# Kernel tuning notes

Hardware: AMD Instinct MI355X
Metric: run time of the kernel (lower is better)

Reference implementation:

```python
import jax, jax.numpy as jnp
import numpy as np

V, S, D, H, F, LYR, NLAB, B = 30522, 512, 768, 12, 3072, 12, 2, 16
DH = D // H
EPS = 1e-5


def layer_norm(x, scale, bias):
    mu = jnp.mean(x, axis=-1, keepdims=True)
    var = jnp.mean((x - mu) ** 2, axis=-1, keepdims=True)
    return (x - mu) * jax.lax.rsqrt(var + EPS) * scale + bias


def setup_inputs() -> dict:
    key = jax.random.key(0)
    ks = jax.random.split(key, 16)
    sc = 0.02
    inp = {
        "input_ids": jax.random.randint(ks[0], (B, S), 0, V),
        "token_emb": jax.random.normal(ks[1], (V, D), jnp.float32) * sc,
        "pos_emb": jax.random.normal(ks[2], (S, D), jnp.float32) * sc,
        "emb_ln_s": jnp.ones((D,), jnp.float32),
        "emb_ln_b": jnp.zeros((D,), jnp.float32),
        "wq": jax.random.normal(ks[3], (LYR, H, D, DH), jnp.float32) * sc,
        "wk": jax.random.normal(ks[4], (LYR, H, D, DH), jnp.float32) * sc,
        "wv": jax.random.normal(ks[5], (LYR, H, D, DH), jnp.float32) * sc,
        "wo": jax.random.normal(ks[6], (LYR, D, D), jnp.float32) * sc,
        "wo_b": jnp.zeros((LYR, D), jnp.float32),
        "ln1_s": jnp.ones((LYR, D), jnp.float32),
        "ln1_b": jnp.zeros((LYR, D), jnp.float32),
        "ln2_s": jnp.ones((LYR, D), jnp.float32),
        "ln2_b": jnp.zeros((LYR, D), jnp.float32),
        "ff1_w": jax.random.normal(ks[7], (LYR, D, F), jnp.float32) * sc,
        "ff1_b": jnp.zeros((LYR, F), jnp.float32),
        "ff2_w": jax.random.normal(ks[8], (LYR, F, D), jnp.float32) * sc,
        "ff2_b": jnp.zeros((LYR, D), jnp.float32),
        "final_ln_s": jnp.ones((D,), jnp.float32),
        "final_ln_b": jnp.zeros((D,), jnp.float32),
        "clf_w": jax.random.normal(ks[9], (D, NLAB), jnp.float32) * sc,
        "clf_b": jnp.zeros((NLAB,), jnp.float32),
    }
    return inp


def _encoder_block(x, wq, wk, wv, wo, wo_b, ln1_s, ln1_b, ln2_s, ln2_b,
                   ff1_w, ff1_b, ff2_w, ff2_b):
    # pre-LN attention with residual
    h = layer_norm(x, ln1_s, ln1_b)
    q = jnp.einsum("bsd,hde->bhse", h, wq)
    k = jnp.einsum("bsd,hde->bhse", h, wk)
    v = jnp.einsum("bsd,hde->bhse", h, wv)
    scores = jnp.einsum("bhse,bhte->bhst", q, k) / jnp.sqrt(jnp.float32(DH))
    # NOTE: source uses log_softmax (quirk), faithfully preserved
    w = jax.nn.log_softmax(scores, axis=-1)
    ctx = jnp.einsum("bhst,bhte->bhse", w, v)
    ctx = ctx.transpose(0, 2, 1, 3).reshape(x.shape[0], x.shape[1], D)
    x = x + ctx @ wo + wo_b
    # pre-LN FFN with residual (exact GELU as in torch nn.GELU)
    h2 = layer_norm(x, ln2_s, ln2_b)
    ff = jax.nn.gelu(h2 @ ff1_w + ff1_b, approximate=False) @ ff2_w + ff2_b
    return x + ff


def reference(input_ids, token_emb, pos_emb, emb_ln_s, emb_ln_b,
              wq, wk, wv, wo, wo_b, ln1_s, ln1_b, ln2_s, ln2_b,
              ff1_w, ff1_b, ff2_w, ff2_b, final_ln_s, final_ln_b,
              clf_w, clf_b):
    x = token_emb[input_ids] + pos_emb[None, :, :]
    x = layer_norm(x, emb_ln_s, emb_ln_b)
    for l in range(LYR):
        x = _encoder_block(x, wq[l], wk[l], wv[l], wo[l], wo_b[l],
                           ln1_s[l], ln1_b[l], ln2_s[l], ln2_b[l],
                           ff1_w[l], ff1_b[l], ff2_w[l], ff2_b[l])
    x = layer_norm(x, final_ln_s, final_ln_b)
    cls = x[:, 0, :]
    return cls @ clf_w + clf_b
```

## Files before the change

### kernel.cpp

```cpp
#include <hip/hip_runtime.h>
#include <hip/hip_bf16.h>
#include <math.h>

typedef __bf16 bf16_t;
typedef __attribute__((ext_vector_type(8))) __bf16 bf16x8;
typedef __attribute__((ext_vector_type(4))) float f32x4;

typedef const __attribute__((address_space(1))) void av1_void;
typedef __attribute__((address_space(3))) void av3_void;

#define DEV static __device__ __forceinline__

DEV void gload16(const void* g, void* l) {
  __builtin_amdgcn_global_load_lds((av1_void*)g, (av3_void*)l, 16, 0, 0);
}

DEV float bsum3(float v, float* red) {
#pragma unroll
  for (int o = 32; o > 0; o >>= 1) v += __shfl_xor(v, o, 64);
  __syncthreads();
  if ((threadIdx.x & 63) == 0) red[threadIdx.x >> 6] = v;
  __syncthreads();
  return red[0] + red[1] + red[2];
}

__global__ __launch_bounds__(192) void k_embed(
    const int* __restrict__ ids, const float* __restrict__ tok,
    const float* __restrict__ pos, const float* __restrict__ gam,
    const float* __restrict__ bet, const float* __restrict__ gam2,
    const float* __restrict__ bet2, float* __restrict__ x,
    bf16_t* __restrict__ h) {
  __shared__ float red[3];
  int row = blockIdx.x;
  int s = row & 511;
  int t = threadIdx.x;
  int id = ids[row];
  const float4 tv = *(const float4*)&tok[(size_t)id * 768 + t * 4];
  const float4 pv = *(const float4*)&pos[(size_t)s * 768 + t * 4];
  float v[4] = {tv.x + pv.x, tv.y + pv.y, tv.z + pv.z, tv.w + pv.w};
  float tot = bsum3(v[0] + v[1] + v[2] + v[3], red);
  float mu = tot * (1.f / 768.f);
  float sq = 0.f;
#pragma unroll
  for (int u = 0; u < 4; ++u) { float d = v[u] - mu; sq += d * d; }
  float var = bsum3(sq, red) * (1.f / 768.f);
  float rstd = rsqrtf(var + 1e-5f);
  const float4 g4 = *(const float4*)&gam[t * 4];
  const float4 b4 = *(const float4*)&bet[t * 4];
  float o[4];
  o[0] = (v[0] - mu) * rstd * g4.x + b4.x;
  o[1] = (v[1] - mu) * rstd * g4.y + b4.y;
  o[2] = (v[2] - mu) * rstd * g4.z + b4.z;
  o[3] = (v[3] - mu) * rstd * g4.w + b4.w;
  float4 ov = {o[0], o[1], o[2], o[3]};
  *(float4*)&x[(size_t)row * 768 + t * 4] = ov;
  float tot2 = bsum3(o[0] + o[1] + o[2] + o[3], red);
  float mu2 = tot2 * (1.f / 768.f);
  float sq2 = 0.f;
#pragma unroll
  for (int u = 0; u < 4; ++u) { float d = o[u] - mu2; sq2 += d * d; }
  float var2 = bsum3(sq2, red) * (1.f / 768.f);
  float rstd2 = rsqrtf(var2 + 1e-5f);
  const float4 G = *(const float4*)&gam2[t * 4];
  const float4 Bb = *(const float4*)&bet2[t * 4];
  union { bf16_t ob[4]; uint2 u2; } pk;
  pk.ob[0] = (bf16_t)((o[0] - mu2) * rstd2 * G.x + Bb.x);
  pk.ob[1] = (bf16_t)((o[1] - mu2) * rstd2 * G.y + Bb.y);
  pk.ob[2] = (bf16_t)((o[2] - mu2) * rstd2 * G.z + Bb.z);
  pk.ob[3] = (bf16_t)((o[3] - mu2) * rstd2 * G.w + Bb.w);
  *(uint2*)&h[(size_t)row * 768 + t * 4] = pk.u2;
}

__global__ __launch_bounds__(256) void k_ln(
    const float* __restrict__ xin, bf16_t* __restrict__ hout,
    const float* __restrict__ gam, const float* __restrict__ bet) {
  int row = blockIdx.x * 4 + (threadIdx.x >> 6);
  int lane = threadIdx.x & 63;
  const float* xr = xin + (size_t)row * 768 + lane * 12;
  float4 a = *(const float4*)&xr[0];
  float4 b = *(const float4*)&xr[4];
  float4 c = *(const float4*)&xr[8];
  float v[12] = {a.x, a.y, a.z, a.w, b.x, b.y, b.z, b.w, c.x, c.y, c.z, c.w};
  float sm = 0.f;
#pragma unroll
  for (int u = 0; u < 12; ++u) sm += v[u];
#pragma unroll
  for (int o = 32; o > 0; o >>= 1) sm += __shfl_xor(sm, o, 64);
  float mu = sm * (1.f / 768.f);
  float sq = 0.f;
#pragma unroll
  for (int u = 0; u < 12; ++u) { float d = v[u] - mu; sq += d * d; }
#pragma unroll
  for (int o = 32; o > 0; o >>= 1) sq += __shfl_xor(sq, o, 64);
  float rstd = rsqrtf(sq * (1.f / 768.f) + 1e-5f);
  const float4 ga = *(const float4*)&gam[lane * 12];
  const float4 gb = *(const float4*)&gam[lane * 12 + 4];
  const float4 gc = *(const float4*)&gam[lane * 12 + 8];
  const float4 ba = *(const float4*)&bet[lane * 12];
  const float4 bb = *(const float4*)&bet[lane * 12 + 4];
  const float4 bc = *(const float4*)&bet[lane * 12 + 8];
  float g[12] = {ga.x, ga.y, ga.z, ga.w, gb.x, gb.y, gb.z, gb.w,
                 gc.x, gc.y, gc.z, gc.w};
  float be[12] = {ba.x, ba.y, ba.z, ba.w, bb.x, bb.y, bb.z, bb.w,
                  bc.x, bc.y, bc.z, bc.w};
  union { bf16_t o[12]; uint2 u2[3]; } pk;
#pragma unroll
  for (int u = 0; u < 12; ++u)
    pk.o[u] = (bf16_t)((v[u] - mu) * rstd * g[u] + be[u]);
  bf16_t* hr = hout + (size_t)row * 768 + lane * 12;
#pragma unroll
  for (int u = 0; u < 3; ++u) *(uint2*)&hr[u * 4] = pk.u2[u];
}

__global__ __launch_bounds__(256) void k_convT(
    const float* __restrict__ in, size_t in_slice, bf16_t* __restrict__ out,
    size_t out_slice, int N, int K) {
  __shared__ float tbuf[32][33];
  int slice = blockIdx.z;
  const float* ip = in + (size_t)slice * in_slice;
  bf16_t* op = out + (size_t)slice * out_slice;
  int n0 = blockIdx.x * 32, k0 = blockIdx.y * 32;
  int c = threadIdx.x & 31, r8 = threadIdx.x >> 5;
#pragma unroll
  for (int i = 0; i < 4; ++i) {
    int rr = r8 + i * 8;
    tbuf[rr][c] = ip[(size_t)(k0 + rr) * N + n0 + c];
  }
  __syncthreads();
#pragma unroll
  for (int i = 0; i < 4; ++i) {
    int rr = r8 + i * 8;
    op[(size_t)(n0 + rr) * K + k0 + c] = (bf16_t)tbuf[c][rr];
  }
}

__global__ __launch_bounds__(256) void k_convT3(
    const float* __restrict__ wq, const float* __restrict__ wk,
    const float* __restrict__ wv, bf16_t* __restrict__ out,
    size_t in_lstride, size_t out_lstride) {
  __shared__ float tbuf[32][33];
  int z = blockIdx.z;
  int l = z / 36, r = z % 36;
  int which = r / 12, head = r % 12;
  const float* ip = (which == 0 ? wq : which == 1 ? wk : wv) +
                    (size_t)l * in_lstride + (size_t)head * 768 * 64;
  bf16_t* op = out + (size_t)l * out_lstride + (size_t)which * 768 * 768 +
               (size_t)head * 64 * 768;
  int n0 = blockIdx.x * 32, k0 = blockIdx.y * 32;
  int c = threadIdx.x & 31, r8 = threadIdx.x >> 5;
#pragma unroll
  for (int i = 0; i < 4; ++i) {
    int rr = r8 + i * 8;
    tbuf[rr][c] = ip[(size_t)(k0 + rr) * 64 + n0 + c];
  }
  __syncthreads();
#pragma unroll
  for (int i = 0; i < 4; ++i) {
    int rr = r8 + i * 8;
    op[(size_t)(n0 + rr) * 768 + k0 + c] = (bf16_t)tbuf[c][rr];
  }
}

template <int EPI>
__global__ __launch_bounds__(256) void k_gemm1(
    const bf16_t* __restrict__ A, int lda, const bf16_t* __restrict__ Bt,
    int ldb, int K, float* __restrict__ Cf, bf16_t* __restrict__ Cb, int ldc,
    const float* __restrict__ bias, int gx) {
  __shared__ __attribute__((aligned(16))) bf16_t As[128 * 64];
  __shared__ __attribute__((aligned(16))) bf16_t Bs[128 * 64];
  const int nwg = gridDim.x;
  const int bid = blockIdx.x;
  const int cpx = nwg >> 3;
  const int swz = (bid & 7) * cpx + (bid >> 3);
  const int bx = swz % gx, by = swz / gx;
  const int m0 = by << 7, n0 = bx << 7;
  const int tid = threadIdx.x;
  const int lane = tid & 63, w = tid >> 6;
  const int wm = w >> 1, wn = w & 1;
  const int r = lane & 15, g4 = lane >> 4;

  f32x4 acc[4][4];
#pragma unroll
  for (int m = 0; m < 4; ++m)
#pragma unroll
    for (int n = 0; n < 4; ++n)
#pragma unroll
      for (int e = 0; e < 4; ++e) acc[m][n][e] = 0.f;

  const bf16_t* pa[4];
  const bf16_t* pb[4];
  char* la[4];
  char* lb[4];
#pragma unroll
  for (int u = 0; u < 4; ++u) {
    int s = u * 256 + tid;
    int row = s >> 3;
    int c = (s & 7) ^ (row & 7);
    pa[u] = A + (size_t)(m0 + row) * lda + c * 8;
    pb[u] = Bt + (size_t)(n0 + row) * ldb + c * 8;
    la[u] = (char*)As + (size_t)(u * 256 + (w << 6)) * 16;
    lb[u] = (char*)Bs + (size_t)(u * 256 + (w << 6)) * 16;
  }

  const int NT = K >> 6;
  for (int t = 0; t < NT; ++t) {
    const int k0 = t << 6;
#pragma unroll
    for (int u = 0; u < 4; ++u) gload16(pa[u] + k0, la[u]);
#pragma unroll
    for (int u = 0; u < 4; ++u) gload16(pb[u] + k0, lb[u]);
    __syncthreads();

#pragma unroll
    for (int kk = 0; kk < 2; ++kk) {
      bf16x8 af[4], bb[4];
#pragma unroll
      for (int m = 0; m < 4; ++m) {
        int row = wm * 64 + m * 16 + r;
        af[m] = *(const bf16x8*)&As[row * 64 +
                                    (((kk << 2) + g4) ^ (row & 7)) * 8];
      }
#pragma unroll
      for (int n = 0; n < 4; ++n) {
        int row = wn * 64 + n * 16 + r;
        bb[n] = *(const bf16x8*)&Bs[row * 64 +
                                    (((kk << 2) + g4) ^ (row & 7)) * 8];
      }
#pragma unroll
      for (int m = 0; m < 4; ++m)
#pragma unroll
        for (int n = 0; n < 4; ++n)
          acc[m][n] = __builtin_amdgcn_mfma_f32_16x16x32_bf16(af[m], bb[n],
                                                              acc[m][n], 0, 0, 0);
    }
    __syncthreads();
  }

#pragma unroll
  for (int m = 0; m < 4; ++m) {
#pragma unroll
    for (int n = 0; n < 4; ++n) {
      int col = n0 + wn * 64 + n * 16 + r;
      float bv = 0.f;
      if constexpr (EPI != 0) bv = bias[col];
#pragma unroll
      for (int j = 0; j < 4; ++j) {
        int row = m0 + wm * 64 + m * 16 + g4 * 4 + j;
        float v = acc[m][n][j];
        if constexpr (EPI == 0) {
          Cb[(size_t)row * ldc + col] = (bf16_t)v;
        } else if constexpr (EPI == 1) {
          size_t o = (size_t)row * ldc + col;
          Cf[o] += v + bv;
        } else {
          float tt = v + bv;
          float ge = 0.5f * tt * (1.f + erff(tt * 0.70710678118f));
          Cb[(size_t)row * ldc + col] = (bf16_t)ge;
        }
      }
    }
  }
}

template <int EPI>
__global__ __launch_bounds__(256) void k_gemm3h(
    const bf16_t* __restrict__ A, int lda, const bf16_t* __restrict__ Bt,
    int ldb, int K, float* __restrict__ Cf, bf16_t* __restrict__ Cb, int ldc,
    const float* __restrict__ bias, int gx) {
  __shared__ __attribute__((aligned(16))) bf16_t As[3][64 * 32];
  __shared__ __attribute__((aligned(16))) bf16_t Bs[3][128 * 32];
  const int nwg = gridDim.x;
  const int bid = blockIdx.x;
  const int cpx = nwg >> 3;
  const int swz = (bid & 7) * cpx + (bid >> 3);
  const int bx = swz % gx, by = swz / gx;
  const int m0 = by << 6, n0 = bx << 7;
  const int tid = threadIdx.x;
  const int lane = tid & 63, w = tid >> 6;
  const int wm = w >> 1, wn = w & 1;
  const int r = lane & 15, g4 = lane >> 4;

  f32x4 acc[2][4];
#pragma unroll
  for (int m = 0; m < 2; ++m)
#pragma unroll
    for (int n = 0; n < 4; ++n)
#pragma unroll
      for (int e = 0; e < 4; ++e) acc[m][n][e] = 0.f;

  const bf16_t* pa0;
  const bf16_t* pb[2];
  uint32_t loa, lob[2];
  {
    int s = tid;
    int row = s >> 2;
    int c = (s & 3) ^ ((row >> 1) & 3);
    pa0 = A + (size_t)(m0 + row) * lda + c * 8;
    loa = (uint32_t)(w << 6) * 16;
#pragma unroll
    for (int u = 0; u < 2; ++u) {
      int sb = u * 256 + tid;
      int rowb = sb >> 2;
      int cb = (sb & 3) ^ ((rowb >> 1) & 3);
      pb[u] = Bt + (size_t)(n0 + rowb) * ldb + cb * 8;
      lob[u] = (uint32_t)(u * 256 + (w << 6)) * 16;
    }
  }

  const int NT = K >> 5;
  auto STAGE = [&](int t, int bufi) {
    int k0 = (t < NT ? t : NT - 1) << 5;
    gload16(pa0 + k0, (char*)&As[bufi][0] + loa);
#pragma unroll
    for (int u = 0; u < 2; ++u) gload16(pb[u] + k0, (char*)&Bs[bufi][0] + lob[u]);
  };

  STAGE(0, 0);
  STAGE(1, 1);
  int bi = 0, si = 2;
  const int co = (g4 ^ ((r >> 1) & 3)) << 3;
  for (int t = 0; t < NT; ++t) {
    asm volatile("s_waitcnt vmcnt(3)" ::: "memory");
    asm volatile("s_barrier" ::: "memory");
    bf16x8 af[2], bb[4];
#pragma unroll
    for (int m = 0; m < 2; ++m) {
      int row = wm * 32 + m * 16 + r;
      af[m] = *(const bf16x8*)&As[bi][row * 32 + co];
    }
#pragma unroll
    for (int n = 0; n < 4; ++n) {
      int row = wn * 64 + n * 16 + r;
      bb[n] = *(const bf16x8*)&Bs[bi][row * 32 + co];
    }
#pragma unroll
    for (int m = 0; m < 2; ++m)
#pragma unroll
      for (int n = 0; n < 4; ++n)
        acc[m][n] = __builtin_amdgcn_mfma_f32_16x16x32_bf16(af[m], bb[n],
                                                            acc[m][n], 0, 0, 0);
    asm volatile("s_barrier" ::: "memory");
    STAGE(t + 2, si);
    si = bi;
    bi = (bi == 2) ? 0 : bi + 1;
  }
  asm volatile("s_waitcnt vmcnt(0)" ::: "memory");

#pragma unroll
  for (int m = 0; m < 2; ++m) {
#pragma unroll
    for (int n = 0; n < 4; ++n) {
      int col = n0 + wn * 64 + n * 16 + r;
      float bv = 0.f;
      if constexpr (EPI != 0) bv = bias[col];
#pragma unroll
      for (int j = 0; j < 4; ++j) {
        int row = m0 + wm * 32 + m * 16 + g4 * 4 + j;
        float v = acc[m][n][j];
        if constexpr (EPI == 0) {
          Cb[(size_t)row * ldc + col] = (bf16_t)v;
        } else if constexpr (EPI == 1) {
          size_t o = (size_t)row * ldc + col;
          Cf[o] += v + bv;
        } else {
          float tt = v + bv;
          float ge = 0.5f * tt * (1.f + erff(tt * 0.70710678118f));
          Cb[(size_t)row * ldc + col] = (bf16_t)ge;
        }
      }
    }
  }
}

__global__ __launch_bounds__(512) void k_attn(const bf16_t* __restrict__ qkv,
                                              bf16_t* __restrict__ ctx) {
  __shared__ __attribute__((aligned(16))) bf16_t Ks[512 * 64];
  __shared__ __attribute__((aligned(16))) float Vs[128 * 64];
  __shared__ __attribute__((aligned(16))) bf16_t Qs[2][128 * 64];
  __shared__ __attribute__((aligned(16))) bf16_t Mt[64 * 64];
  __shared__ float svp[8 * 64];
  __shared__ float svs[64];

  int bh = blockIdx.x;
  int b = bh / 12, hh = bh % 12;
  int tid = threadIdx.x, lane = tid & 63, w = tid >> 6;
  int r = lane & 15, g4 = lane >> 4;
  const bf16_t* qb = qkv + (size_t)b * 512 * 2304 + hh * 64;
  const bf16_t* kb = qb + 768;
  const bf16_t* vb = qb + 1536;

#pragma unroll
  for (int i = 0; i < 8; ++i) {
    int s = i * 512 + tid;
    int row = s >> 3;
    int c = (s & 7) ^ (row & 7);
    gload16(kb + (size_t)row * 2304 + c * 8,
            (char*)Ks + (size_t)(i * 512 + (w << 6)) * 16);
  }

  f32x4 macc[2];
#pragma unroll
  for (int jj = 0; jj < 2; ++jj)
#pragma unroll
    for (int e = 0; e < 4; ++e) macc[jj][e] = 0.f;
  float svacc = 0.f;
  const int e1hi = (lane >> 3), e1lo = (lane & 7);

  bf16x8 vreg[2];
  auto ldV = [&](int t0) {
#pragma unroll
    for (int i = 0; i < 2; ++i) {
      int cs = i * 512 + tid;
      int row = cs >> 3, col = (cs & 7) * 8;
      vreg[i] = *(const bf16x8*)(vb + (size_t)(t0 + row) * 2304 + col);
    }
  };
  auto wrV = [&]() {
#pragma unroll
    for (int i = 0; i < 2; ++i) {
      int cs = i * 512 + tid;
      int row = cs >> 3, col = (cs & 7) * 8;
      f32x4 v0, v1;
#pragma unroll
      for (int u = 0; u < 4; ++u) {
        v0[u] = (float)vreg[i][u];
        v1[u] = (float)vreg[i][u + 4];
      }
      *(f32x4*)&Vs[row * 64 + col] = v0;
      *(f32x4*)&Vs[row * 64 + col + 4] = v1;
    }
  };

  ldV(0);
  wrV();
  __syncthreads();

  for (int t0 = 0; t0 < 4; ++t0) {
    if (t0 < 3) ldV((t0 + 1) * 128);
#pragma unroll 8
    for (int tt = 0; tt < 128; ++tt) {
      int t = t0 * 128 + tt;
      float kv = (float)Ks[t * 64 + (((e1hi ^ (t & 7)) << 3) | e1lo)];
#pragma unroll
      for (int jj = 0; jj < 2; ++jj) {
        f32x4 vv = *(const f32x4*)&Vs[tt * 64 + w * 8 + jj * 4];
        macc[jj] += kv * vv;
      }
    }
#pragma unroll
    for (int q = 0; q < 16; ++q)
      svacc += Vs[((w << 4) + q) * 64 + lane];
    __syncthreads();
    if (t0 < 3) {
      wrV();
      __syncthreads();
    }
  }

#pragma unroll
  for (int jj = 0; jj < 2; ++jj)
#pragma unroll
    for (int u = 0; u < 4; ++u) {
      int e2 = w * 8 + jj * 4 + u;
      Mt[e2 * 64 + (((e1hi ^ (e2 & 7)) << 3) | e1lo)] =
          (bf16_t)(macc[jj][u] * 0.125f);
    }
  svp[w * 64 + lane] = svacc;
  __syncthreads();
  if (w == 0) {
    float s = 0.f;
#pragma unroll
    for (int u = 0; u < 8; ++u) s += svp[u * 64 + lane];
    svs[lane] = s;
  }

  auto stageQ = [&](int qc, int bufi) {
#pragma unroll
    for (int u = 0; u < 2; ++u) {
      int s = u * 512 + tid;
      int row = s >> 3;
      int c = (s & 7) ^ (row & 7);
      gload16(qb + (size_t)(qc * 128 + row) * 2304 + c * 8,
              (char*)&Qs[bufi][0] + (size_t)(u * 512 + (w << 6)) * 16);
    }
  };
  stageQ(0, 0);
  const int arow = w * 16 + r;

  for (int qc = 0; qc < 4; ++qc) {
    __syncthreads();
    if (qc < 3) stageQ(qc + 1, (qc + 1) & 1);
    const bf16_t* Qb = &Qs[qc & 1][0];

    f32x4 acc2[32];
#pragma unroll
    for (int n = 0; n < 32; ++n)
#pragma unroll
      for (int e = 0; e < 4; ++e) acc2[n][e] = 0.f;

#pragma unroll
    for (int kk = 0; kk < 2; ++kk) {
      bf16x8 aq = *(const bf16x8*)&Qb[arow * 64 +
                                      (((kk << 2) + g4) ^ (arow & 7)) * 8];
#pragma unroll
      for (int n = 0; n < 32; ++n) {
        int krow = n * 16 + r;
        bf16x8 bk = *(const bf16x8*)&Ks[krow * 64 +
                                        (((kk << 2) + g4) ^ (krow & 7)) * 8];
        acc2[n] = __builtin_amdgcn_mfma_f32_16x16x32_bf16(aq, bk, acc2[n], 0, 0, 0);
      }
    }

    float lse_j[4];
#pragma unroll
    for (int j = 0; j < 4; ++j) {
      float mx = -1e30f;
#pragma unroll
      for (int n = 0; n < 32; ++n) mx = fmaxf(mx, acc2[n][j] * 0.125f);
#pragma unroll
      for (int o = 1; o < 16; o <<= 1) mx = fmaxf(mx, __shfl_xor(mx, o, 64));
      float sm = 0.f;
#pragma unroll
      for (int n = 0; n < 32; ++n) sm += __expf(acc2[n][j] * 0.125f - mx);
#pragma unroll
      for (int o = 1; o < 16; o <<= 1) sm += __shfl_xor(sm, o, 64);
      lse_j[j] = mx + __logf(sm);
    }

    f32x4 acc3[4];
#pragma unroll
    for (int n = 0; n < 4; ++n)
#pragma unroll
      for (int e = 0; e < 4; ++e) acc3[n][e] = 0.f;
#pragma unroll
    for (int kk = 0; kk < 2; ++kk) {
      bf16x8 aq = *(const bf16x8*)&Qb[arow * 64 +
                                      (((kk << 2) + g4) ^ (arow & 7)) * 8];
#pragma unroll
      for (int n2 = 0; n2 < 4; ++n2) {
        int mrow = n2 * 16 + r;
        bf16x8 bm = *(const bf16x8*)&Mt[mrow * 64 +
                                        (((kk << 2) + g4) ^ (mrow & 7)) * 8];
        acc3[n2] = __builtin_amdgcn_mfma_f32_16x16x32_bf16(aq, bm, acc3[n2], 0, 0, 0);
      }
    }
#pragma unroll
    for (int n2 = 0; n2 < 4; ++n2) {
      int col = n2 * 16 + r;
      float svv = svs[col];
#pragma unroll
      for (int j = 0; j < 4; ++j) {
        int srow = qc * 128 + w * 16 + g4 * 4 + j;
        ctx[((size_t)(b * 512 + srow)) * 768 + hh * 64 + col] =
            (bf16_t)(acc3[n2][j] - lse_j[j] * svv);
      }
    }
  }
}

__global__ __launch_bounds__(192) void k_final(
    const float* __restrict__ x, const float* __restrict__ gam,
    const float* __restrict__ bet, const float* __restrict__ cw,
    const float* __restrict__ cb, float* __restrict__ out) {
  __shared__ float red[3];
  int b = blockIdx.x, t = threadIdx.x;
  const float* xr = x + (size_t)b * 512 * 768;
  const float4 xv = *(const float4*)&xr[t * 4];
  float v[4] = {xv.x, xv.y, xv.z, xv.w};
  float tot = bsum3(v[0] + v[1] + v[2] + v[3], red);
  float mu = tot * (1.f / 768.f);
  float sq = 0.f;
#pragma unroll
  for (int u = 0; u < 4; ++u) { float d = v[u] - mu; sq += d * d; }
  float var = bsum3(sq, red) * (1.f / 768.f);
  float rstd = rsqrtf(var + 1e-5f);
  const float4 g4 = *(const float4*)&gam[t * 4];
  const float4 b4 = *(const float4*)&bet[t * 4];
  float nv[4];
  nv[0] = (v[0] - mu) * rstd * g4.x + b4.x;
  nv[1] = (v[1] - mu) * rstd * g4.y + b4.y;
  nv[2] = (v[2] - mu) * rstd * g4.z + b4.z;
  nv[3] = (v[3] - mu) * rstd * g4.w + b4.w;
  const float4 wa = *(const float4*)&cw[t * 8];
  const float4 wb = *(const float4*)&cw[t * 8 + 4];
  float d0 = nv[0] * wa.x + nv[1] * wa.z + nv[2] * wb.x + nv[3] * wb.z;
  float d1 = nv[0] * wa.y + nv[1] * wa.w + nv[2] * wb.y + nv[3] * wb.w;
  d0 = bsum3(d0, red);
  d1 = bsum3(d1, red);
  if (t == 0) {
    out[b * 2 + 0] = d0 + cb[0];
    out[b * 2 + 1] = d1 + cb[1];
  }
}

static constexpr size_t OFF_X = 0;
static constexpr size_t OFF_H = OFF_X + 8192ull * 768 * 4;
static constexpr size_t OFF_QG = OFF_H + 8192ull * 768 * 2;
static constexpr size_t OFF_CTX = OFF_QG + 8192ull * 3072 * 2;
static constexpr size_t OFF_LSE = OFF_CTX + 8192ull * 768 * 2;
static constexpr size_t OFF_W = OFF_LSE + 192ull * 512 * 4;
static constexpr size_t WPL = 7077888;
static constexpr size_t WS_SMALL = OFF_W + WPL * 2;
static constexpr size_t WS_BIG = OFF_W + 12ull * WPL * 2;

extern "C" void kernel_launch(void* const* d_in, const int* in_sizes, int n_in,
                              void* d_out, int out_size, void* d_ws,
                              size_t ws_size, hipStream_t stream) {
  const int* ids = (const int*)d_in[0];
  const float* tok = (const float*)d_in[1];
  const float* pos = (const float*)d_in[2];
  const float* eln_s = (const float*)d_in[3];
  const float* eln_b = (const float*)d_in[4];
  const float* wq = (const float*)d_in[5];
  const float* wk = (const float*)d_in[6];
  const float* wv = (const float*)d_in[7];
  const float* wo = (const float*)d_in[8];
  const float* wo_b = (const float*)d_in[9];
  const float* ln1_s = (const float*)d_in[10];
  const float* ln1_b = (const float*)d_in[11];
  const float* ln2_s = (const float*)d_in[12];
  const float* ln2_b = (const float*)d_in[13];
  const float* ff1w = (const float*)d_in[14];
  const float* ff1b = (const float*)d_in[15];
  const float* ff2w = (const float*)d_in[16];
  const float* ff2b = (const float*)d_in[17];
  const float* fln_s = (const float*)d_in[18];
  const float* fln_b = (const float*)d_in[19];
  const float* cw = (const float*)d_in[20];
  const float* cb = (const float*)d_in[21];
  float* out = (float*)d_out;

  if (ws_size < WS_SMALL) return;
  const bool big = ws_size >= WS_BIG;

  char* ws = (char*)d_ws;
  float* x = (float*)(ws + OFF_X);
  bf16_t* h = (bf16_t*)(ws + OFF_H);
  bf16_t* qkv = (bf16_t*)(ws + OFF_QG);
  bf16_t* gbuf = (bf16_t*)(ws + OFF_QG);
  bf16_t* ctx = (bf16_t*)(ws + OFF_CTX);
  bf16_t* wT = (bf16_t*)(ws + OFF_W);

  k_embed<<<8192, 192, 0, stream>>>(ids, tok, pos, eln_s, eln_b,
                                    ln1_s, ln1_b, x, h);

  if (big) {
    k_convT3<<<dim3(2, 24, 432), 256, 0, stream>>>(wq, wk, wv, wT,
                                                   589824, WPL);
    k_convT<<<dim3(24, 24, 12), 256, 0, stream>>>(wo, 589824,
                                                  wT + 1769472, WPL, 768, 768);
    k_convT<<<dim3(96, 24, 12), 256, 0, stream>>>(ff1w, 2359296,
                                                  wT + 2359296, WPL, 3072, 768);
    k_convT<<<dim3(24, 96, 12), 256, 0, stream>>>(ff2w, 2359296,
                                                  wT + 4718592, WPL, 768, 3072);
  }

  for (int l = 0; l < 12; ++l) {
    bf16_t* wl = big ? wT + (size_t)l * WPL : wT;
    bf16_t* qkvT = wl;
    bf16_t* woT = wl + 1769472;
    bf16_t* ff1T = wl + 2359296;
    bf16_t* ff2T = wl + 4718592;

    if (l > 0)
      k_ln<<<2048, 256, 0, stream>>>(x, h, ln1_s + l * 768, ln1_b + l * 768);
    if (!big) {
      k_convT3<<<dim3(2, 24, 36), 256, 0, stream>>>(
          wq + (size_t)l * 589824, wk + (size_t)l * 589824,
          wv + (size_t)l * 589824, qkvT, 589824, 0);
      k_convT<<<dim3(24, 24, 1), 256, 0, stream>>>(wo + (size_t)l * 589824, 0,
                                                   woT, 0, 768, 768);
      k_convT<<<dim3(96, 24, 1), 256, 0, stream>>>(ff1w + (size_t)l * 2359296,
                                                   0, ff1T, 0, 3072, 768);
      k_convT<<<dim3(24, 96, 1), 256, 0, stream>>>(ff2w + (size_t)l * 2359296,
                                                   0, ff2T, 0, 768, 3072);
    }
    k_gemm1<0><<<1152, 256, 0, stream>>>(h, 768, qkvT, 768, 768,
                                         nullptr, qkv, 2304, nullptr, 18);
    k_attn<<<192, 512, 0, stream>>>(qkv, ctx);
    k_gemm3h<1><<<768, 256, 0, stream>>>(ctx, 768, woT, 768, 768, x,
                                         nullptr, 768, wo_b + l * 768, 6);
    k_ln<<<2048, 256, 0, stream>>>(x, h, ln2_s + l * 768, ln2_b + l * 768);
    k_gemm1<2><<<1536, 256, 0, stream>>>(h, 768, ff1T, 768, 768,
                                         nullptr, gbuf, 3072,
                                         ff1b + l * 3072, 24);
    k_gemm3h<1><<<768, 256, 0, stream>>>(gbuf, 3072, ff2T, 3072, 3072, x,
                                         nullptr, 768, ff2b + l * 768, 6);
  }
  k_final<<<16, 192, 0, stream>>>(x, fln_s, fln_b, cw, cb, out);
}
```

Before: 3.397 ms.

## Store residual stream in bf16 and interleave QK and PV MFMAs in attention

The fp32 residual stream x becomes bf16 in the embed, layernorm, GEMM residual-add epilogues and final kernel. This halves the bytes read and written for the residual on every layer. It also adds a rounding step on every residual accumulation across 12 layers, which can cost accuracy. Separately, the attention kernel now issues the value-product MFMAs in the same loop as the score MFMAs, before the log-sum-exp reduction, so one Q fragment load serves both.

```diff
diff --git a/kernel.cpp b/kernel.cpp
--- a/kernel.cpp
+++ b/kernel.cpp
@@ -14,6 +14,8 @@
 DEV void gload16(const void* g, void* l) {
   __builtin_amdgcn_global_load_lds((av1_void*)g, (av3_void*)l, 16, 0, 0);
 }
+
+DEV float b2f(bf16_t v) { return (float)v; }
 
 DEV float bsum3(float v, float* red) {
 #pragma unroll
@@ -28,7 +30,7 @@
     const int* __restrict__ ids, const float* __restrict__ tok,
     const float* __restrict__ pos, const float* __restrict__ gam,
     const float* __restrict__ bet, const float* __restrict__ gam2,
-    const float* __restrict__ bet2, float* __restrict__ x,
+    const float* __restrict__ bet2, bf16_t* __restrict__ x,
     bf16_t* __restrict__ h) {
   __shared__ float red[3];
   int row = blockIdx.x;
@@ -52,35 +54,41 @@
   o[1] = (v[1] - mu) * rstd * g4.y + b4.y;
   o[2] = (v[2] - mu) * rstd * g4.z + b4.z;
   o[3] = (v[3] - mu) * rstd * g4.w + b4.w;
-  float4 ov = {o[0], o[1], o[2], o[3]};
-  *(float4*)&x[(size_t)row * 768 + t * 4] = ov;
-  float tot2 = bsum3(o[0] + o[1] + o[2] + o[3], red);
+  union { bf16_t ob[4]; uint2 u2; } px;
+  px.ob[0] = (bf16_t)o[0]; px.ob[1] = (bf16_t)o[1];
+  px.ob[2] = (bf16_t)o[2]; px.ob[3] = (bf16_t)o[3];
+  *(uint2*)&x[(size_t)row * 768 + t * 4] = px.u2;
+  float q[4] = {b2f(px.ob[0]), b2f(px.ob[1]), b2f(px.ob[2]), b2f(px.ob[3])};
+  float tot2 = bsum3(q[0] + q[1] + q[2] + q[3], red);
   float mu2 = tot2 * (1.f / 768.f);
   float sq2 = 0.f;
 #pragma unroll
-  for (int u = 0; u < 4; ++u) { float d = o[u] - mu2; sq2 += d * d; }
+  for (int u = 0; u < 4; ++u) { float d = q[u] - mu2; sq2 += d * d; }
   float var2 = bsum3(sq2, red) * (1.f / 768.f);
   float rstd2 = rsqrtf(var2 + 1e-5f);
   const float4 G = *(const float4*)&gam2[t * 4];
   const float4 Bb = *(const float4*)&bet2[t * 4];
   union { bf16_t ob[4]; uint2 u2; } pk;
-  pk.ob[0] = (bf16_t)((o[0] - mu2) * rstd2 * G.x + Bb.x);
-  pk.ob[1] = (bf16_t)((o[1] - mu2) * rstd2 * G.y + Bb.y);
-  pk.ob[2] = (bf16_t)((o[2] - mu2) * rstd2 * G.z + Bb.z);
-  pk.ob[3] = (bf16_t)((o[3] - mu2) * rstd2 * G.w + Bb.w);
+  pk.ob[0] = (bf16_t)((q[0] - mu2) * rstd2 * G.x + Bb.x);
+  pk.ob[1] = (bf16_t)((q[1] - mu2) * rstd2 * G.y + Bb.y);
+  pk.ob[2] = (bf16_t)((q[2] - mu2) * rstd2 * G.z + Bb.z);
+  pk.ob[3] = (bf16_t)((q[3] - mu2) * rstd2 * G.w + Bb.w);
   *(uint2*)&h[(size_t)row * 768 + t * 4] = pk.u2;
 }
 
 __global__ __launch_bounds__(256) void k_ln(
-    const float* __restrict__ xin, bf16_t* __restrict__ hout,
+    const bf16_t* __restrict__ xin, bf16_t* __restrict__ hout,
     const float* __restrict__ gam, const float* __restrict__ bet) {
   int row = blockIdx.x * 4 + (threadIdx.x >> 6);
   int lane = threadIdx.x & 63;
-  const float* xr = xin + (size_t)row * 768 + lane * 12;
-  float4 a = *(const float4*)&xr[0];
-  float4 b = *(const float4*)&xr[4];
-  float4 c = *(const float4*)&xr[8];
-  float v[12] = {a.x, a.y, a.z, a.w, b.x, b.y, b.z, b.w, c.x, c.y, c.z, c.w};
+  const bf16_t* xr = xin + (size_t)row * 768 + lane * 12;
+  union { uint2 u; bf16_t h[4]; } ua, ub, uc;
+  ua.u = *(const uint2*)&xr[0];
+  ub.u = *(const uint2*)&xr[4];
+  uc.u = *(const uint2*)&xr[8];
+  float v[12] = {b2f(ua.h[0]), b2f(ua.h[1]), b2f(ua.h[2]), b2f(ua.h[3]),
+                 b2f(ub.h[0]), b2f(ub.h[1]), b2f(ub.h[2]), b2f(ub.h[3]),
+                 b2f(uc.h[0]), b2f(uc.h[1]), b2f(uc.h[2]), b2f(uc.h[3])};
   float sm = 0.f;
 #pragma unroll
   for (int u = 0; u < 12; ++u) sm += v[u];
@@ -164,7 +172,7 @@
 template <int EPI>
 __global__ __launch_bounds__(256) void k_gemm1(
     const bf16_t* __restrict__ A, int lda, const bf16_t* __restrict__ Bt,
-    int ldb, int K, float* __restrict__ Cf, bf16_t* __restrict__ Cb, int ldc,
+    int ldb, int K, bf16_t* __restrict__ Cf, bf16_t* __restrict__ Cb, int ldc,
     const float* __restrict__ bias, int gx) {
   __shared__ __attribute__((aligned(16))) bf16_t As[128 * 64];
   __shared__ __attribute__((aligned(16))) bf16_t Bs[128 * 64];
@@ -251,7 +259,7 @@
           Cb[(size_t)row * ldc + col] = (bf16_t)v;
         } else if constexpr (EPI == 1) {
           size_t o = (size_t)row * ldc + col;
-          Cf[o] += v + bv;
+          Cf[o] = (bf16_t)(b2f(Cf[o]) + v + bv);
         } else {
           float tt = v + bv;
           float ge = 0.5f * tt * (1.f + erff(tt * 0.70710678118f));
@@ -265,7 +273,7 @@
 template <int EPI>
 __global__ __launch_bounds__(256) void k_gemm3h(
     const bf16_t* __restrict__ A, int lda, const bf16_t* __restrict__ Bt,
-    int ldb, int K, float* __restrict__ Cf, bf16_t* __restrict__ Cb, int ldc,
+    int ldb, int K, bf16_t* __restrict__ Cf, bf16_t* __restrict__ Cb, int ldc,
     const float* __restrict__ bias, int gx) {
   __shared__ __attribute__((aligned(16))) bf16_t As[3][64 * 32];
   __shared__ __attribute__((aligned(16))) bf16_t Bs[3][128 * 32];
@@ -361,7 +369,7 @@
           Cb[(size_t)row * ldc + col] = (bf16_t)v;
         } else if constexpr (EPI == 1) {
           size_t o = (size_t)row * ldc + col;
-          Cf[o] += v + bv;
+          Cf[o] = (bf16_t)(b2f(Cf[o]) + v + bv);
         } else {
           float tt = v + bv;
           float ge = 0.5f * tt * (1.f + erff(tt * 0.70710678118f));
@@ -493,10 +501,15 @@
     const bf16_t* Qb = &Qs[qc & 1][0];
 
     f32x4 acc2[32];
+    f32x4 acc3[4];
 #pragma unroll
     for (int n = 0; n < 32; ++n)
 #pragma unroll
       for (int e = 0; e < 4; ++e) acc2[n][e] = 0.f;
+#pragma unroll
+    for (int n = 0; n < 4; ++n)
+#pragma unroll
+      for (int e = 0; e < 4; ++e) acc3[n][e] = 0.f;
 
 #pragma unroll
     for (int kk = 0; kk < 2; ++kk) {
@@ -509,33 +522,6 @@
                                         (((kk << 2) + g4) ^ (krow & 7)) * 8];
         acc2[n] = __builtin_amdgcn_mfma_f32_16x16x32_bf16(aq, bk, acc2[n], 0, 0, 0);
       }
-    }
-
-    float lse_j[4];
-#pragma unroll
-    for (int j = 0; j < 4; ++j) {
-      float mx = -1e30f;
-#pragma unroll
-      for (int n = 0; n < 32; ++n) mx = fmaxf(mx, acc2[n][j] * 0.125f);
-#pragma unroll
-      for (int o = 1; o < 16; o <<= 1) mx = fmaxf(mx, __shfl_xor(mx, o, 64));
-      float sm = 0.f;
-#pragma unroll
-      for (int n = 0; n < 32; ++n) sm += __expf(acc2[n][j] * 0.125f - mx);
-#pragma unroll
-      for (int o = 1; o < 16; o <<= 1) sm += __shfl_xor(sm, o, 64);
-      lse_j[j] = mx + __logf(sm);
-    }
-
-    f32x4 acc3[4];
-#pragma unroll
-    for (int n = 0; n < 4; ++n)
-#pragma unroll
-      for (int e = 0; e < 4; ++e) acc3[n][e] = 0.f;
-#pragma unroll
-    for (int kk = 0; kk < 2; ++kk) {
-      bf16x8 aq = *(const bf16x8*)&Qb[arow * 64 +
-                                      (((kk << 2) + g4) ^ (arow & 7)) * 8];
 #pragma unroll
       for (int n2 = 0; n2 < 4; ++n2) {
         int mrow = n2 * 16 + r;
@@ -544,6 +530,23 @@
         acc3[n2] = __builtin_amdgcn_mfma_f32_16x16x32_bf16(aq, bm, acc3[n2], 0, 0, 0);
       }
     }
+
+    float lse_j[4];
+#pragma unroll
+    for (int j = 0; j < 4; ++j) {
+      float mx = -1e30f;
+#pragma unroll
+      for (int n = 0; n < 32; ++n) mx = fmaxf(mx, acc2[n][j] * 0.125f);
+#pragma unroll
+      for (int o = 1; o < 16; o <<= 1) mx = fmaxf(mx, __shfl_xor(mx, o, 64));
+      float sm = 0.f;
+#pragma unroll
+      for (int n = 0; n < 32; ++n) sm += __expf(acc2[n][j] * 0.125f - mx);
+#pragma unroll
+      for (int o = 1; o < 16; o <<= 1) sm += __shfl_xor(sm, o, 64);
+      lse_j[j] = mx + __logf(sm);
+    }
+
 #pragma unroll
     for (int n2 = 0; n2 < 4; ++n2) {
       int col = n2 * 16 + r;
@@ -559,14 +562,15 @@
 }
 
 __global__ __launch_bounds__(192) void k_final(
-    const float* __restrict__ x, const float* __restrict__ gam,
+    const bf16_t* __restrict__ x, const float* __restrict__ gam,
     const float* __restrict__ bet, const float* __restrict__ cw,
     const float* __restrict__ cb, float* __restrict__ out) {
   __shared__ float red[3];
   int b = blockIdx.x, t = threadIdx.x;
-  const float* xr = x + (size_t)b * 512 * 768;
-  const float4 xv = *(const float4*)&xr[t * 4];
-  float v[4] = {xv.x, xv.y, xv.z, xv.w};
+  const bf16_t* xr = x + (size_t)b * 512 * 768;
+  union { uint2 u; bf16_t h[4]; } ux;
+  ux.u = *(const uint2*)&xr[t * 4];
+  float v[4] = {b2f(ux.h[0]), b2f(ux.h[1]), b2f(ux.h[2]), b2f(ux.h[3])};
   float tot = bsum3(v[0] + v[1] + v[2] + v[3], red);
   float mu = tot * (1.f / 768.f);
   float sq = 0.f;
@@ -634,7 +638,7 @@
   const bool big = ws_size >= WS_BIG;
 
   char* ws = (char*)d_ws;
-  float* x = (float*)(ws + OFF_X);
+  bf16_t* x = (bf16_t*)(ws + OFF_X);
   bf16_t* h = (bf16_t*)(ws + OFF_H);
   bf16_t* qkv = (bf16_t*)(ws + OFF_QG);
   bf16_t* gbuf = (bf16_t*)(ws + OFF_QG);
```

Measured after the change: 3.308 ms, median of 2. 1.03x faster.
